# Kernel tuning notes

Hardware: AMD Instinct MI355X
Metric: run time of the kernel (lower is better)

Reference implementation:

```python
import math
import jax, jax.numpy as jnp
import numpy as np

NODE_DIM = 256
EDGE_DIM = 64
NUM_HEADS = 8
ATTN_DIM = NODE_DIM // NUM_HEADS


def setup_inputs() -> dict:
    key = jax.random.key(0)
    ks = jax.random.split(key, 12)
    B, N = 2, 256
    s_node = 1.0 / math.sqrt(NODE_DIM)
    s_edge = 1.0 / math.sqrt(EDGE_DIM)
    return {
        "nodes": jax.random.normal(ks[0], (B, N, NODE_DIM), jnp.float32),
        "edges": jax.random.normal(ks[1], (B, N, N, EDGE_DIM), jnp.float32),
        "W_qkv": jax.random.normal(ks[2], (NODE_DIM, 3 * NODE_DIM), jnp.float32) * s_node,
        "b_qkv": jax.random.normal(ks[3], (3 * NODE_DIM,), jnp.float32) * 0.01,
        "W_ss": jax.random.normal(ks[4], (EDGE_DIM, 2 * NODE_DIM), jnp.float32) * s_edge,
        "b_ss": jax.random.normal(ks[5], (2 * NODE_DIM,), jnp.float32) * 0.01,
        "W_nodes": jax.random.normal(ks[6], (NODE_DIM, NODE_DIM), jnp.float32) * s_node,
        "b_nodes": jax.random.normal(ks[7], (NODE_DIM,), jnp.float32) * 0.01,
        "W_edges": jax.random.normal(ks[8], (NODE_DIM, EDGE_DIM), jnp.float32) * s_node,
        "b_edges": jax.random.normal(ks[9], (EDGE_DIM,), jnp.float32) * 0.01,
    }


def reference(nodes, edges, W_qkv, b_qkv, W_ss, b_ss, W_nodes, b_nodes, W_edges, b_edges):
    B, N, _ = nodes.shape
    H, D = NUM_HEADS, ATTN_DIM

    qkv = nodes @ W_qkv + b_qkv                      # [B,N,3*node_dim]
    q, k, v = jnp.split(qkv, 3, axis=-1)
    q = q.reshape(B, N, H, D).transpose(0, 2, 1, 3)  # [B,H,N,D]
    k = k.reshape(B, N, H, D).transpose(0, 2, 1, 3)
    v = v.reshape(B, N, H, D).transpose(0, 2, 1, 3)

    # explicit outer product: [B,H,Nq,Nk,D]
    attn = q[:, :, :, None, :] * k[:, :, None, :, :]

    ss = edges @ W_ss + b_ss                         # [B,N,N,2*node_dim]
    shift, scale = jnp.split(ss, 2, axis=-1)
    shift = shift.reshape(B, N, N, H, D).transpose(0, 3, 1, 2, 4)  # [B,H,N,N,D]
    scale = scale.reshape(B, N, N, H, D).transpose(0, 3, 1, 2, 4)

    new_edges = attn * scale + attn + shift          # [B,H,Nq,Nk,D]

    logits = new_edges.sum(axis=4) / math.sqrt(D)    # [B,H,Nq,Nk]
    # NOTE: original softmaxes over dim=2 (the query axis) — reproduced faithfully
    attention = jax.nn.softmax(logits, axis=2)

    # intended math of `attention @ values` then head-merge
    weighted = jnp.einsum('bhqk,bhkd->bqhd', attention, v).reshape(B, N, H * D)

    edge_feat = new_edges.transpose(0, 2, 3, 1, 4).reshape(B, N, N, H * D)

    new_nodes = weighted @ W_nodes + b_nodes
    new_edges_out = jax.nn.leaky_relu(edge_feat, negative_slope=0.1) @ W_edges + b_edges
    return new_nodes, new_edges_out
```

## Files before the change

kernel.cpp:

```cpp
#include <hip/hip_runtime.h>


typedef unsigned short ushortT;
typedef short s16x8 __attribute__((ext_vector_type(8)));
typedef float f32x4 __attribute__((ext_vector_type(4)));

#define MFMA16(a, b, c) __builtin_amdgcn_mfma_f32_16x16x32_bf16(a, b, c, 0, 0, 0)

#define CF4(p) (*reinterpret_cast<const float4*>(p))
#define CF2(p) (*reinterpret_cast<const float2*>(p))
#define F4(p)  (*reinterpret_cast<float4*>(p))
#define F2(p)  (*reinterpret_cast<float2*>(p))

__device__ __forceinline__ ushortT f2bf(float x) {
  union { float f; unsigned u; } v; v.f = x;
  unsigned r = (v.u + 0x7FFFu + ((v.u >> 16) & 1u)) >> 16;
  return (ushortT)r;
}
__device__ __forceinline__ float bf2f(ushortT h) {
  union { unsigned u; float f; } v; v.u = ((unsigned)h) << 16;
  return v.f;
}

__device__ __forceinline__ void gemm32_body(
    const float* __restrict__ A, const float* __restrict__ B,
    const float* __restrict__ bias, float* __restrict__ C,
    int Nn, int K, int blk)
{
  __shared__ float As[16][36];
  __shared__ float Bs[16][68];
  const int t  = threadIdx.x;
  const int nbx = Nn >> 6;
  const int bx = blk % nbx;
  const int by = blk / nbx;
  const int r0 = by << 5, c0 = bx << 6;
  const int tx = t & 15, ty = t >> 4;
  float acc[2][4];
#pragma unroll
  for (int i = 0; i < 2; ++i)
#pragma unroll
    for (int j = 0; j < 4; ++j) acc[i][j] = 0.f;

  for (int kt = 0; kt < K; kt += 16) {
    {
      const int r = t >> 3, k2 = (t & 7) << 1;
      const float2 a = CF2(A + (size_t)(r0 + r) * K + kt + k2);
      As[k2 + 0][r] = a.x; As[k2 + 1][r] = a.y;
    }
    {
      const int kk = t >> 4, c4 = (t & 15) << 2;
      F4(&Bs[kk][c4]) = CF4(B + (size_t)(kt + kk) * Nn + c0 + c4);
    }
    __syncthreads();
#pragma unroll
    for (int kk = 0; kk < 16; ++kk) {
      const float a0 = As[kk][ty * 2 + 0];
      const float a1 = As[kk][ty * 2 + 1];
      const float4 bv = F4(&Bs[kk][tx << 2]);
      const float bb[4] = {bv.x, bv.y, bv.z, bv.w};
#pragma unroll
      for (int cc = 0; cc < 4; ++cc) {
        acc[0][cc] = fmaf(a0, bb[cc], acc[0][cc]);
        acc[1][cc] = fmaf(a1, bb[cc], acc[1][cc]);
      }
    }
    __syncthreads();
  }
  const float4 bv = CF4(bias + c0 + (tx << 2));
  const float bb[4] = {bv.x, bv.y, bv.z, bv.w};
#pragma unroll
  for (int rr = 0; rr < 2; ++rr) {
    float4 o;
    o.x = acc[rr][0] + bb[0]; o.y = acc[rr][1] + bb[1];
    o.z = acc[rr][2] + bb[2]; o.w = acc[rr][3] + bb[3];
    F4(C + (size_t)(r0 + ty * 2 + rr) * Nn + c0 + (tx << 2)) = o;
  }
}

__global__ __launch_bounds__(256) void qkv_prep_kernel(
    const float* __restrict__ nodes, const float* __restrict__ W_qkv,
    const float* __restrict__ b_qkv, float* __restrict__ qkv,
    const float* __restrict__ W_ss, const float* __restrict__ W_edges,
    ushortT* __restrict__ WssT_h, ushortT* __restrict__ WssT_l,
    ushortT* __restrict__ WeT_h,  ushortT* __restrict__ WeT_l)
{
  if (blockIdx.x < 192) {
    gemm32_body(nodes, W_qkv, b_qkv, qkv, 768, 256, blockIdx.x);
    return;
  }
  const int idx = (blockIdx.x - 192) * 256 + threadIdx.x;
  for (int e = idx; e < 512 * 64; e += 16384) {
    const int c = e >> 6, i = e & 63;
    const float x = W_ss[i * 512 + c];
    const ushortT h = f2bf(x);
    WssT_h[e] = h;
    WssT_l[e] = f2bf(x - bf2f(h));
  }
  for (int e = idx; e < 64 * 256; e += 16384) {
    const int j = e >> 8, c = e & 255;
    const float x = W_edges[c * 64 + j];
    const ushortT h = f2bf(x);
    WeT_h[e] = h;
    WeT_l[e] = f2bf(x - bf2f(h));
  }
}

__global__ __launch_bounds__(256) void gemm32_kernel(
    const float* __restrict__ A, const float* __restrict__ B,
    const float* __restrict__ bias, float* __restrict__ C, int Nn, int K)
{
  gemm32_body(A, B, bias, C, Nn, K, blockIdx.x);
}

__global__ __launch_bounds__(256, 2) void edge_mfma_kernel(
    const float* __restrict__ edges, const float* __restrict__ qkv,
    const ushortT* __restrict__ WssT_h, const ushortT* __restrict__ WssT_l,
    const float* __restrict__ b_ss,
    const ushortT* __restrict__ WeT_h, const ushortT* __restrict__ WeT_l,
    const float* __restrict__ b_edges,
    float* __restrict__ out_edges, float* __restrict__ logits)
{
  __shared__ __align__(16) char pool[70656];
  ushortT* Eh = (ushortT*)pool;
  ushortT* El = (ushortT*)(pool + 16384);
  float* lgbuf = (float*)(pool + 65536);
  float* qv_l  = (float*)(pool + 69632 - 4096 + 4096);
  qv_l = (float*)(pool + 69632);

  const int t    = threadIdx.x;
  const int lane = t & 63;
  const int w    = t >> 6;
  const int l15  = lane & 15;
  const int lg   = lane >> 4;
  const int bid  = blockIdx.x;
  const int kh   = bid & 1;
  const int q    = (bid >> 1) & 255;
  const int b    = bid >> 9;
  const int k0   = kh << 7;
  const int rw   = w << 5;

  qv_l[t] = qkv[(size_t)(b * 256 + q) * 768 + t];

  const float* eBase = edges + ((size_t)((b * 256 + q) * 256 + k0)) * 64;
#pragma unroll
  for (int u = 0; u < 8; ++u) {
    const int f = t + u * 256;
    const int r = f >> 4, i4 = (f & 15) << 2;
    const float4 v = CF4(eBase + r * 64 + i4);
    const ushortT h0 = f2bf(v.x), h1 = f2bf(v.y), h2 = f2bf(v.z), h3 = f2bf(v.w);
    const ushortT e0 = f2bf(v.x - bf2f(h0)), e1 = f2bf(v.y - bf2f(h1)),
                  e2 = f2bf(v.z - bf2f(h2)), e3 = f2bf(v.w - bf2f(h3));
    int byte = r * 128 + i4 * 2; byte ^= (r & 7) << 4;
    *reinterpret_cast<ushort4*>((char*)Eh + byte) = make_ushort4(h0, h1, h2, h3);
    *reinterpret_cast<ushort4*>((char*)El + byte) = make_ushort4(e0, e1, e2, e3);
  }

  const f32x4 zero4 = {0.f, 0.f, 0.f, 0.f};
  f32x4 accO[2][4];
#pragma unroll
  for (int rt = 0; rt < 2; ++rt)
#pragma unroll
    for (int jt = 0; jt < 4; ++jt) accO[rt][jt] = zero4;

  for (int ch = 0; ch < 4; ++ch) {
    const int c0 = ch << 6;

    __syncthreads();
    {
      const ushortT* srcs[4] = {
        WssT_h + (size_t)c0 * 64, WssT_h + 16384 + (size_t)c0 * 64,
        WssT_l + (size_t)c0 * 64, WssT_l + 16384 + (size_t)c0 * 64 };
#pragma unroll
      for (int part = 0; part < 4; ++part) {
#pragma unroll
        for (int it = 0; it < 2; ++it) {
          const int id = t + it * 256;
          const int cc = id >> 3, k8 = (id & 7) << 3;
          int dbyte = 32768 + part * 8192 + cc * 128 + k8 * 2;
          dbyte ^= (cc & 7) << 4;
          *reinterpret_cast<s16x8*>(pool + dbyte) =
              *reinterpret_cast<const s16x8*>(srcs[part] + cc * 64 + k8);
        }
      }
    }
    __syncthreads();

    float kvreg[2][4][4];
#pragma unroll
    for (int rt = 0; rt < 2; ++rt)
#pragma unroll
      for (int ct = 0; ct < 4; ++ct) {
        const float* kvp = qkv + (size_t)(b * 256 + k0 + rw + rt * 16 + lg * 4) * 768
                               + 256 + c0 + ct * 16 + l15;
#pragma unroll
        for (int r = 0; r < 4; ++r) kvreg[rt][ct][r] = kvp[(size_t)r * 768];
      }

    f32x4 accS[2][4], accC[2][4];
#pragma unroll
    for (int ct = 0; ct < 4; ++ct) {
      const float bs = b_ss[c0 + ct * 16 + l15];
      const float bc = b_ss[256 + c0 + ct * 16 + l15];
      const f32x4 vs = {bs, bs, bs, bs}, vc = {bc, bc, bc, bc};
      accS[0][ct] = vs; accS[1][ct] = vs;
      accC[0][ct] = vc; accC[1][ct] = vc;
    }
#pragma unroll
    for (int ks = 0; ks < 2; ++ks) {
      s16x8 ah[2], al[2];
#pragma unroll
      for (int rt = 0; rt < 2; ++rt) {
        const int row = rw + rt * 16 + l15;
        int abyte = row * 128 + (32 * ks + 8 * lg) * 2; abyte ^= (row & 7) << 4;
        ah[rt] = *reinterpret_cast<const s16x8*>((const char*)Eh + abyte);
        al[rt] = *reinterpret_cast<const s16x8*>((const char*)El + abyte);
      }
#pragma unroll
      for (int ct = 0; ct < 4; ++ct) {
        const int cc = ct * 16 + l15;
        int wb = 32768 + cc * 128 + (32 * ks + 8 * lg) * 2; wb ^= (cc & 7) << 4;
        const s16x8 bsh = *reinterpret_cast<const s16x8*>(pool + wb);
        const s16x8 bch = *reinterpret_cast<const s16x8*>(pool + wb + 8192);
        const s16x8 bsl = *reinterpret_cast<const s16x8*>(pool + wb + 16384);
        const s16x8 bcl = *reinterpret_cast<const s16x8*>(pool + wb + 24576);
#pragma unroll
        for (int rt = 0; rt < 2; ++rt) {
          accS[rt][ct] = MFMA16(ah[rt], bsh, accS[rt][ct]);
          accS[rt][ct] = MFMA16(ah[rt], bsl, accS[rt][ct]);
          accS[rt][ct] = MFMA16(al[rt], bsh, accS[rt][ct]);
          accC[rt][ct] = MFMA16(ah[rt], bch, accC[rt][ct]);
          accC[rt][ct] = MFMA16(ah[rt], bcl, accC[rt][ct]);
          accC[rt][ct] = MFMA16(al[rt], bch, accC[rt][ct]);
        }
      }
    }
    __syncthreads();

    float lgacc[2][2][4];
#pragma unroll
    for (int rt = 0; rt < 2; ++rt)
#pragma unroll
      for (int hh = 0; hh < 2; ++hh)
#pragma unroll
        for (int r = 0; r < 4; ++r) lgacc[rt][hh][r] = 0.f;

#pragma unroll
    for (int rt = 0; rt < 2; ++rt) {
#pragma unroll
      for (int ct = 0; ct < 4; ++ct) {
        const float qvc = qv_l[c0 + ct * 16 + l15];
#pragma unroll
        for (int r = 0; r < 4; ++r) {
          const float a  = qvc * kvreg[rt][ct][r];
          const float ne = fmaf(a, accC[rt][ct][r], a) + accS[rt][ct][r];
          lgacc[rt][ct >> 1][r] += ne;
          const float nel = ne > 0.f ? ne : 0.1f * ne;
          const ushortT nh = f2bf(nel);
          const ushortT nl = f2bf(nel - bf2f(nh));
          const int row = rw + rt * 16 + lg * 4 + r;
          int byte = row * 128 + (ct * 16 + l15) * 2; byte ^= (row & 7) << 4;
          *reinterpret_cast<ushortT*>(pool + 32768 + byte) = nh;
          *reinterpret_cast<ushortT*>(pool + 49152 + byte) = nl;
        }
      }
    }

#pragma unroll
    for (int rt = 0; rt < 2; ++rt)
#pragma unroll
      for (int hh = 0; hh < 2; ++hh)
#pragma unroll
        for (int r = 0; r < 4; ++r) {
          float v = lgacc[rt][hh][r];
          v += __shfl_xor(v, 1);
          v += __shfl_xor(v, 2);
          v += __shfl_xor(v, 4);
          v += __shfl_xor(v, 8);
          lgacc[rt][hh][r] = v;
        }
    if (l15 == 0) {
#pragma unroll
      for (int rt = 0; rt < 2; ++rt)
#pragma unroll
        for (int hh = 0; hh < 2; ++hh)
#pragma unroll
          for (int r = 0; r < 4; ++r)
            lgbuf[(ch * 2 + hh) * 128 + rw + rt * 16 + lg * 4 + r] = lgacc[rt][hh][r];
    }

#pragma unroll
    for (int ks = 0; ks < 2; ++ks) {
      s16x8 anh[2], anl[2];
#pragma unroll
      for (int rt = 0; rt < 2; ++rt) {
        const int row = rw + rt * 16 + l15;
        int abyte = row * 128 + (32 * ks + 8 * lg) * 2; abyte ^= (row & 7) << 4;
        anh[rt] = *reinterpret_cast<const s16x8*>(pool + 32768 + abyte);
        anl[rt] = *reinterpret_cast<const s16x8*>(pool + 49152 + abyte);
      }
#pragma unroll
      for (int jt = 0; jt < 4; ++jt) {
        const size_t off = (size_t)(jt * 16 + l15) * 256 + c0 + 32 * ks + 8 * lg;
        const s16x8 wh = *reinterpret_cast<const s16x8*>(WeT_h + off);
        const s16x8 wl = *reinterpret_cast<const s16x8*>(WeT_l + off);
#pragma unroll
        for (int rt = 0; rt < 2; ++rt) {
          accO[rt][jt] = MFMA16(anh[rt], wh, accO[rt][jt]);
          accO[rt][jt] = MFMA16(anh[rt], wl, accO[rt][jt]);
          accO[rt][jt] = MFMA16(anl[rt], wh, accO[rt][jt]);
        }
      }
    }
  }

  __syncthreads();
  float* outb = (float*)pool;
#pragma unroll
  for (int rt = 0; rt < 2; ++rt)
#pragma unroll
    for (int jt = 0; jt < 4; ++jt) {
      const float be = b_edges[jt * 16 + l15];
#pragma unroll
      for (int r = 0; r < 4; ++r) {
        const int row = rw + rt * 16 + lg * 4 + r;
        outb[row * 68 + jt * 16 + l15] = accO[rt][jt][r] + be;
      }
    }
  __syncthreads();
  {
    float* oBase = out_edges + ((size_t)((b * 256 + q) * 256 + k0)) * 64;
#pragma unroll
    for (int u = 0; u < 8; ++u) {
      const int idx = t + u * 256;
      const int row = idx >> 4, c4 = (idx & 15) << 2;
      float4 o;
      o.x = outb[row * 68 + c4 + 0]; o.y = outb[row * 68 + c4 + 1];
      o.z = outb[row * 68 + c4 + 2]; o.w = outb[row * 68 + c4 + 3];
      F4(oBase + (size_t)row * 64 + c4) = o;
    }
    const int h = t >> 5, i4 = (t & 31) << 2;
    const float s = 0.17677669529663687f;
    float4 o;
    o.x = lgbuf[h * 128 + i4 + 0] * s; o.y = lgbuf[h * 128 + i4 + 1] * s;
    o.z = lgbuf[h * 128 + i4 + 2] * s; o.w = lgbuf[h * 128 + i4 + 3] * s;
    F4(logits + ((size_t)((b * 8 + h) * 256 + q)) * 256 + k0 + i4) = o;
  }
}

__global__ __launch_bounds__(256) void softmax_stats_kernel(
    const float* __restrict__ logits, float* __restrict__ mOut, float* __restrict__ rOut)
{
  __shared__ float sm[8][33], sx[8][33];
  const int bh = blockIdx.x >> 3, kc = blockIdx.x & 7;
  const int kl = threadIdx.x & 31, qg = threadIdx.x >> 5;
  const float* base = logits + (size_t)bh * 65536 + kc * 32 + kl;
  float arr[32];
#pragma unroll
  for (int i = 0; i < 32; ++i) arr[i] = base[(size_t)(qg * 32 + i) * 256];
  float m = arr[0];
#pragma unroll
  for (int i = 1; i < 32; ++i) m = fmaxf(m, arr[i]);
  float s = 0.f;
#pragma unroll
  for (int i = 0; i < 32; ++i) s += __expf(arr[i] - m);
  sm[qg][kl] = m; sx[qg][kl] = s;
  __syncthreads();
  if (threadIdx.x < 32) {
    float M = sm[0][kl];
#pragma unroll
    for (int g = 1; g < 8; ++g) M = fmaxf(M, sm[g][kl]);
    float S = 0.f;
#pragma unroll
    for (int g = 0; g < 8; ++g) S += sx[g][kl] * __expf(sm[g][kl] - M);
    mOut[bh * 256 + kc * 32 + kl] = M;
    rOut[bh * 256 + kc * 32 + kl] = 1.f / S;
  }
}

__global__ __launch_bounds__(256) void weighted_fused_kernel(
    const float* __restrict__ logits, const float* __restrict__ mOut,
    const float* __restrict__ rOut, const float* __restrict__ qkv,
    float* __restrict__ weighted)
{
  __shared__ float P[16][260];
  __shared__ float mc[256], rc[256];
  const int qt = blockIdx.x & 15, h = (blockIdx.x >> 4) & 7, b = blockIdx.x >> 7;
  const int bh = b * 8 + h;
  const int t = threadIdx.x;
  mc[t] = mOut[bh * 256 + t];
  rc[t] = rOut[bh * 256 + t];
  __syncthreads();
  const float* lb = logits + (size_t)bh * 65536 + (size_t)qt * 16 * 256;
#pragma unroll
  for (int u = 0; u < 4; ++u) {
    const int f = t + u * 256;
    const int qq = f >> 6, k4 = (f & 63) << 2;
    const float4 v = CF4(lb + qq * 256 + k4);
    P[qq][k4 + 0] = __expf(v.x - mc[k4 + 0]) * rc[k4 + 0];
    P[qq][k4 + 1] = __expf(v.y - mc[k4 + 1]) * rc[k4 + 1];
    P[qq][k4 + 2] = __expf(v.z - mc[k4 + 2]) * rc[k4 + 2];
    P[qq][k4 + 3] = __expf(v.w - mc[k4 + 3]) * rc[k4 + 3];
  }
  __syncthreads();
  const int dd = t & 15, qq = t >> 4;
  const float* vb = qkv + (size_t)b * 196608 + 512 + h * 32 + dd * 2;
  float a0 = 0.f, a1 = 0.f;
#pragma unroll 8
  for (int k = 0; k < 256; ++k) {
    const float p = P[qq][k];
    const float2 v = CF2(vb + (size_t)k * 768);
    a0 = fmaf(p, v.x, a0); a1 = fmaf(p, v.y, a1);
  }
  float2 o; o.x = a0; o.y = a1;
  F2(weighted + ((size_t)(b * 256 + qt * 16 + qq)) * 256 + h * 32 + dd * 2) = o;
}

extern "C" void kernel_launch(void* const* d_in, const int* in_sizes, int n_in,
                              void* d_out, int out_size, void* d_ws, size_t ws_size,
                              hipStream_t stream) {
  const float* nodes   = (const float*)d_in[0];
  const float* edges   = (const float*)d_in[1];
  const float* W_qkv   = (const float*)d_in[2];
  const float* b_qkv   = (const float*)d_in[3];
  const float* W_ss    = (const float*)d_in[4];
  const float* b_ss    = (const float*)d_in[5];
  const float* W_nodes = (const float*)d_in[6];
  const float* b_nodes = (const float*)d_in[7];
  const float* W_edges = (const float*)d_in[8];
  const float* b_edges = (const float*)d_in[9];

  float* out_nodes = (float*)d_out;
  float* out_edges = out_nodes + 131072;

  float* wsf      = (float*)d_ws;
  float* qkv      = wsf;
  float* logits   = wsf + 393216;
  float* weighted = wsf + 1441792;
  float* mcol     = wsf + 1572864;
  float* rcol     = wsf + 1576960;
  ushortT* wss    = (ushortT*)(wsf + 1581056);
  ushortT* WssT_h = wss;
  ushortT* WssT_l = wss + 32768;
  ushortT* WeT_h  = wss + 65536;
  ushortT* WeT_l  = wss + 81920;

  qkv_prep_kernel<<<256, 256, 0, stream>>>(nodes, W_qkv, b_qkv, qkv,
                                           W_ss, W_edges, WssT_h, WssT_l, WeT_h, WeT_l);
  edge_mfma_kernel<<<1024, 256, 0, stream>>>(edges, qkv, WssT_h, WssT_l, b_ss,
                                             WeT_h, WeT_l, b_edges, out_edges, logits);
  softmax_stats_kernel<<<128, 256, 0, stream>>>(logits, mcol, rcol);
  weighted_fused_kernel<<<256, 256, 0, stream>>>(logits, mcol, rcol, qkv, weighted);
  gemm32_kernel<<<64, 256, 0, stream>>>(weighted, W_nodes, b_nodes, out_nodes, 256, 256);
}
```

Baseline: 227.7 us.

## Keep edge fragments in registers and read W_ss from global to cut LDS

The edge tile is converted to bf16 hi/lo fragments directly in registers instead of being staged through shared memory. The W_ss chunks are read per column tile straight from global or L2 rather than copied into LDS. The output staging buffer now uses an XOR swizzle instead of padding. Together these shrink LDS from about 69 KB to 37 KB and drop several barriers, allowing three blocks per CU, at the cost of higher register pressure and more global/L2 weight traffic.

```diff
diff --git a/kernel.cpp b/kernel.cpp
--- a/kernel.cpp
+++ b/kernel.cpp
@@ -112,7 +112,7 @@
   gemm32_body(A, B, bias, C, Nn, K, blockIdx.x);
 }
 
-__global__ __launch_bounds__(256, 2) void edge_mfma_kernel(
+__global__ __launch_bounds__(256, 3) void edge_mfma_kernel(
     const float* __restrict__ edges, const float* __restrict__ qkv,
     const ushortT* __restrict__ WssT_h, const ushortT* __restrict__ WssT_l,
     const float* __restrict__ b_ss,
@@ -120,12 +120,9 @@
     const float* __restrict__ b_edges,
     float* __restrict__ out_edges, float* __restrict__ logits)
 {
-  __shared__ __align__(16) char pool[70656];
-  ushortT* Eh = (ushortT*)pool;
-  ushortT* El = (ushortT*)(pool + 16384);
-  float* lgbuf = (float*)(pool + 65536);
-  float* qv_l  = (float*)(pool + 69632 - 4096 + 4096);
-  qv_l = (float*)(pool + 69632);
+  __shared__ __align__(16) char pool[37888];
+  float* lgbuf = (float*)(pool + 32768);
+  float* qv_l  = (float*)(pool + 36864);
 
   const int t    = threadIdx.x;
   const int lane = t & 63;
@@ -141,19 +138,24 @@
 
   qv_l[t] = qkv[(size_t)(b * 256 + q) * 768 + t];
 
-  const float* eBase = edges + ((size_t)((b * 256 + q) * 256 + k0)) * 64;
-#pragma unroll
-  for (int u = 0; u < 8; ++u) {
-    const int f = t + u * 256;
-    const int r = f >> 4, i4 = (f & 15) << 2;
-    const float4 v = CF4(eBase + r * 64 + i4);
-    const ushortT h0 = f2bf(v.x), h1 = f2bf(v.y), h2 = f2bf(v.z), h3 = f2bf(v.w);
-    const ushortT e0 = f2bf(v.x - bf2f(h0)), e1 = f2bf(v.y - bf2f(h1)),
-                  e2 = f2bf(v.z - bf2f(h2)), e3 = f2bf(v.w - bf2f(h3));
-    int byte = r * 128 + i4 * 2; byte ^= (r & 7) << 4;
-    *reinterpret_cast<ushort4*>((char*)Eh + byte) = make_ushort4(h0, h1, h2, h3);
-    *reinterpret_cast<ushort4*>((char*)El + byte) = make_ushort4(e0, e1, e2, e3);
-  }
+  s16x8 eh[2][2], el[2][2];
+#pragma unroll
+  for (int rt = 0; rt < 2; ++rt)
+#pragma unroll
+    for (int ks = 0; ks < 2; ++ks) {
+      const int row = rw + rt * 16 + l15;
+      const float* ep = edges + ((size_t)((b * 256 + q) * 256 + k0 + row)) * 64
+                              + 32 * ks + 8 * lg;
+      const float4 v0 = CF4(ep), v1 = CF4(ep + 4);
+      const float xs[8] = {v0.x, v0.y, v0.z, v0.w, v1.x, v1.y, v1.z, v1.w};
+#pragma unroll
+      for (int i = 0; i < 8; ++i) {
+        const ushortT h = f2bf(xs[i]);
+        eh[rt][ks][i] = (short)h;
+        el[rt][ks][i] = (short)f2bf(xs[i] - bf2f(h));
+      }
+    }
+  __syncthreads();
 
   const f32x4 zero4 = {0.f, 0.f, 0.f, 0.f};
   f32x4 accO[2][4];
@@ -164,103 +166,68 @@
 
   for (int ch = 0; ch < 4; ++ch) {
     const int c0 = ch << 6;
-
-    __syncthreads();
-    {
-      const ushortT* srcs[4] = {
-        WssT_h + (size_t)c0 * 64, WssT_h + 16384 + (size_t)c0 * 64,
-        WssT_l + (size_t)c0 * 64, WssT_l + 16384 + (size_t)c0 * 64 };
-#pragma unroll
-      for (int part = 0; part < 4; ++part) {
-#pragma unroll
-        for (int it = 0; it < 2; ++it) {
-          const int id = t + it * 256;
-          const int cc = id >> 3, k8 = (id & 7) << 3;
-          int dbyte = 32768 + part * 8192 + cc * 128 + k8 * 2;
-          dbyte ^= (cc & 7) << 4;
-          *reinterpret_cast<s16x8*>(pool + dbyte) =
-              *reinterpret_cast<const s16x8*>(srcs[part] + cc * 64 + k8);
+    float lgacc[2][2][4];
+#pragma unroll
+    for (int rt = 0; rt < 2; ++rt)
+#pragma unroll
+      for (int hh = 0; hh < 2; ++hh)
+#pragma unroll
+        for (int r = 0; r < 4; ++r) lgacc[rt][hh][r] = 0.f;
+
+#pragma unroll
+    for (int ct = 0; ct < 4; ++ct) {
+      const int col = c0 + ct * 16 + l15;
+
+      float kv[2][4];
+#pragma unroll
+      for (int rt = 0; rt < 2; ++rt) {
+        const float* kvp = qkv + (size_t)(b * 256 + k0 + rw + rt * 16 + lg * 4) * 768
+                               + 256 + col;
+#pragma unroll
+        for (int r = 0; r < 4; ++r) kv[rt][r] = kvp[(size_t)r * 768];
+      }
+
+      const float bs = b_ss[col];
+      const float bc = b_ss[256 + col];
+      f32x4 aS[2], aC[2];
+      {
+        const f32x4 vs = {bs, bs, bs, bs}, vc = {bc, bc, bc, bc};
+        aS[0] = vs; aS[1] = vs; aC[0] = vc; aC[1] = vc;
+      }
+
+#pragma unroll
+      for (int ks = 0; ks < 2; ++ks) {
+        const size_t off = (size_t)col * 64 + 32 * ks + 8 * lg;
+        const s16x8 bsh = *reinterpret_cast<const s16x8*>(WssT_h + off);
+        const s16x8 bsl = *reinterpret_cast<const s16x8*>(WssT_l + off);
+        const s16x8 bch = *reinterpret_cast<const s16x8*>(WssT_h + off + 16384);
+        const s16x8 bcl = *reinterpret_cast<const s16x8*>(WssT_l + off + 16384);
+#pragma unroll
+        for (int rt = 0; rt < 2; ++rt) {
+          aS[rt] = MFMA16(eh[rt][ks], bsh, aS[rt]);
+          aS[rt] = MFMA16(eh[rt][ks], bsl, aS[rt]);
+          aS[rt] = MFMA16(el[rt][ks], bsh, aS[rt]);
+          aC[rt] = MFMA16(eh[rt][ks], bch, aC[rt]);
+          aC[rt] = MFMA16(eh[rt][ks], bcl, aC[rt]);
+          aC[rt] = MFMA16(el[rt][ks], bch, aC[rt]);
         }
       }
-    }
-    __syncthreads();
-
-    float kvreg[2][4][4];
-#pragma unroll
-    for (int rt = 0; rt < 2; ++rt)
-#pragma unroll
-      for (int ct = 0; ct < 4; ++ct) {
-        const float* kvp = qkv + (size_t)(b * 256 + k0 + rw + rt * 16 + lg * 4) * 768
-                               + 256 + c0 + ct * 16 + l15;
-#pragma unroll
-        for (int r = 0; r < 4; ++r) kvreg[rt][ct][r] = kvp[(size_t)r * 768];
-      }
-
-    f32x4 accS[2][4], accC[2][4];
-#pragma unroll
-    for (int ct = 0; ct < 4; ++ct) {
-      const float bs = b_ss[c0 + ct * 16 + l15];
-      const float bc = b_ss[256 + c0 + ct * 16 + l15];
-      const f32x4 vs = {bs, bs, bs, bs}, vc = {bc, bc, bc, bc};
-      accS[0][ct] = vs; accS[1][ct] = vs;
-      accC[0][ct] = vc; accC[1][ct] = vc;
-    }
-#pragma unroll
-    for (int ks = 0; ks < 2; ++ks) {
-      s16x8 ah[2], al[2];
+
+      const float qvc = qv_l[col];
 #pragma unroll
       for (int rt = 0; rt < 2; ++rt) {
-        const int row = rw + rt * 16 + l15;
-        int abyte = row * 128 + (32 * ks + 8 * lg) * 2; abyte ^= (row & 7) << 4;
-        ah[rt] = *reinterpret_cast<const s16x8*>((const char*)Eh + abyte);
-        al[rt] = *reinterpret_cast<const s16x8*>((const char*)El + abyte);
-      }
-#pragma unroll
-      for (int ct = 0; ct < 4; ++ct) {
-        const int cc = ct * 16 + l15;
-        int wb = 32768 + cc * 128 + (32 * ks + 8 * lg) * 2; wb ^= (cc & 7) << 4;
-        const s16x8 bsh = *reinterpret_cast<const s16x8*>(pool + wb);
-        const s16x8 bch = *reinterpret_cast<const s16x8*>(pool + wb + 8192);
-        const s16x8 bsl = *reinterpret_cast<const s16x8*>(pool + wb + 16384);
-        const s16x8 bcl = *reinterpret_cast<const s16x8*>(pool + wb + 24576);
-#pragma unroll
-        for (int rt = 0; rt < 2; ++rt) {
-          accS[rt][ct] = MFMA16(ah[rt], bsh, accS[rt][ct]);
-          accS[rt][ct] = MFMA16(ah[rt], bsl, accS[rt][ct]);
-          accS[rt][ct] = MFMA16(al[rt], bsh, accS[rt][ct]);
-          accC[rt][ct] = MFMA16(ah[rt], bch, accC[rt][ct]);
-          accC[rt][ct] = MFMA16(ah[rt], bcl, accC[rt][ct]);
-          accC[rt][ct] = MFMA16(al[rt], bch, accC[rt][ct]);
-        }
-      }
-    }
-    __syncthreads();
-
-    float lgacc[2][2][4];
-#pragma unroll
-    for (int rt = 0; rt < 2; ++rt)
-#pragma unroll
-      for (int hh = 0; hh < 2; ++hh)
-#pragma unroll
-        for (int r = 0; r < 4; ++r) lgacc[rt][hh][r] = 0.f;
-
-#pragma unroll
-    for (int rt = 0; rt < 2; ++rt) {
-#pragma unroll
-      for (int ct = 0; ct < 4; ++ct) {
-        const float qvc = qv_l[c0 + ct * 16 + l15];
 #pragma unroll
         for (int r = 0; r < 4; ++r) {
-          const float a  = qvc * kvreg[rt][ct][r];
-          const float ne = fmaf(a, accC[rt][ct][r], a) + accS[rt][ct][r];
+          const float a  = qvc * kv[rt][r];
+          const float ne = fmaf(a, aC[rt][r], a) + aS[rt][r];
           lgacc[rt][ct >> 1][r] += ne;
           const float nel = ne > 0.f ? ne : 0.1f * ne;
           const ushortT nh = f2bf(nel);
           const ushortT nl = f2bf(nel - bf2f(nh));
           const int row = rw + rt * 16 + lg * 4 + r;
           int byte = row * 128 + (ct * 16 + l15) * 2; byte ^= (row & 7) << 4;
-          *reinterpret_cast<ushortT*>(pool + 32768 + byte) = nh;
-          *reinterpret_cast<ushortT*>(pool + 49152 + byte) = nl;
+          *reinterpret_cast<ushortT*>(pool + byte) = nh;
+          *reinterpret_cast<ushortT*>(pool + 16384 + byte) = nl;
         }
       }
     }
@@ -295,8 +262,8 @@
       for (int rt = 0; rt < 2; ++rt) {
         const int row = rw + rt * 16 + l15;
         int abyte = row * 128 + (32 * ks + 8 * lg) * 2; abyte ^= (row & 7) << 4;
-        anh[rt] = *reinterpret_cast<const s16x8*>(pool + 32768 + abyte);
-        anl[rt] = *reinterpret_cast<const s16x8*>(pool + 49152 + abyte);
+        anh[rt] = *reinterpret_cast<const s16x8*>(pool + abyte);
+        anl[rt] = *reinterpret_cast<const s16x8*>(pool + 16384 + abyte);
       }
 #pragma unroll
       for (int jt = 0; jt < 4; ++jt) {
@@ -314,7 +281,6 @@
   }
 
   __syncthreads();
-  float* outb = (float*)pool;
 #pragma unroll
   for (int rt = 0; rt < 2; ++rt)
 #pragma unroll
@@ -323,7 +289,8 @@
 #pragma unroll
       for (int r = 0; r < 4; ++r) {
         const int row = rw + rt * 16 + lg * 4 + r;
-        outb[row * 68 + jt * 16 + l15] = accO[rt][jt][r] + be;
+        int byte = (row * 64 + jt * 16 + l15) * 4; byte ^= (row & 7) << 4;
+        *reinterpret_cast<float*>(pool + byte) = accO[rt][jt][r] + be;
       }
     }
   __syncthreads();
@@ -333,10 +300,8 @@
     for (int u = 0; u < 8; ++u) {
       const int idx = t + u * 256;
       const int row = idx >> 4, c4 = (idx & 15) << 2;
-      float4 o;
-      o.x = outb[row * 68 + c4 + 0]; o.y = outb[row * 68 + c4 + 1];
-      o.z = outb[row * 68 + c4 + 2]; o.w = outb[row * 68 + c4 + 3];
-      F4(oBase + (size_t)row * 64 + c4) = o;
+      int byte = (row * 64 + c4) * 4; byte ^= (row & 7) << 4;
+      F4(oBase + (size_t)row * 64 + c4) = *reinterpret_cast<float4*>(pool + byte);
     }
     const int h = t >> 5, i4 = (t & 31) << 2;
     const float s = 0.17677669529663687f;
```

New measurement: 334.1 us. +46.8%, slower.
